# Optimization experiments

Measured on AMD Instinct MI355X. Metric: run time of the kernel, lower is better.

Reference implementation:

```python
import jax, jax.numpy as jnp
import numpy as np
from jax import lax

EPS = 1e-5  # BatchNorm eps (torch default)


def _bn_relu_conv3x3_s2(x, bn_w, bn_b, bn_m, bn_v, w, b):
    # eval-mode BatchNorm2d -> ReLU -> conv3x3 stride 2 pad 1 (NCHW)
    inv = bn_w / jnp.sqrt(bn_v + EPS)
    y = x * inv[None, :, None, None] + (bn_b - bn_m * inv)[None, :, None, None]
    y = jax.nn.relu(y)
    y = lax.conv_general_dilated(y, w, window_strides=(2, 2),
                                 padding=((1, 1), (1, 1)),
                                 dimension_numbers=("NCHW", "OIHW", "NCHW"))
    return y + b[None, :, None, None]


def _avgpool2x2(x):
    B, C, H, W = x.shape
    return x.reshape(B, C, H // 2, 2, W // 2, 2).mean(axis=(3, 5))


def setup_inputs() -> dict:
    key = jax.random.key(0)
    ks = jax.random.split(key, 24)
    C, C3 = 128, 128 // 3
    d = {"x": jax.random.normal(ks[0], (8, C, 96, 96), jnp.float32)}
    for i, p in enumerate(["f", "g", "h"]):
        base = 1 + i * 6
        d[p + "_bn_w"] = jax.random.uniform(ks[base], (C,), jnp.float32, 0.5, 1.5)
        d[p + "_bn_b"] = jax.random.normal(ks[base + 1], (C,), jnp.float32) * 0.1
        d[p + "_bn_m"] = jax.random.normal(ks[base + 2], (C,), jnp.float32) * 0.1
        d[p + "_bn_v"] = jax.random.uniform(ks[base + 3], (C,), jnp.float32, 0.5, 1.5)
        d[p + "_w"] = jax.random.normal(ks[base + 4], (C, C, 3, 3), jnp.float32) * (1.0 / np.sqrt(9 * C))
        d[p + "_b"] = jax.random.normal(ks[base + 5], (C,), jnp.float32) * 0.01
    d["se_cw"] = jax.random.normal(ks[19], (C3, 2 * C), jnp.float32) * (1.0 / np.sqrt(2 * C))
    d["se_cb"] = jax.random.normal(ks[20], (C3,), jnp.float32) * 0.01
    d["se_uw"] = jax.random.normal(ks[21], (C, C3), jnp.float32) * (1.0 / np.sqrt(C3))
    d["se_ub"] = jax.random.normal(ks[22], (C,), jnp.float32) * 0.01
    d["gamma"] = jax.random.normal(ks[23], (1,), jnp.float32) * 0.5
    return d


def reference(x, f_bn_w, f_bn_b, f_bn_m, f_bn_v, f_w, f_b,
              g_bn_w, g_bn_b, g_bn_m, g_bn_v, g_w, g_b,
              h_bn_w, h_bn_b, h_bn_m, h_bn_v, h_w, h_b,
              se_cw, se_cb, se_uw, se_ub, gamma):
    B, C, H, W = x.shape
    left = _avgpool2x2(x)  # isPrimary=False branch -> [B,C,H/2,W/2]

    f = _bn_relu_conv3x3_s2(x, f_bn_w, f_bn_b, f_bn_m, f_bn_v, f_w, f_b)
    g = _bn_relu_conv3x3_s2(x, g_bn_w, g_bn_b, g_bn_m, g_bn_v, g_w, g_b)
    h = _bn_relu_conv3x3_s2(x, h_bn_w, h_bn_b, h_bn_m, h_bn_v, h_w, h_b)

    Ho, Wo = f.shape[2], f.shape[3]
    N = Ho * Wo
    ff = f.reshape(B, C, N)
    gg = g.reshape(B, C, N)
    hh = h.reshape(B, C, N)

    # s = softmax over last axis of f^T g : [B, N, N]
    scores = jnp.einsum("bcn,bcm->bnm", ff, gg)
    attn = jax.nn.softmax(scores, axis=2)
    s = jnp.einsum("bcn,bnm->bcm", hh, attn).reshape(B, C, Ho, Wo)
    s = gamma[0] * s

    # CompetitiveSE: global-avg x and s -> concat(2C) -> ReLU/1x1(C//3) -> ReLU/1x1(C)
    wx = x.mean(axis=(2, 3))          # [B, C]
    ws = s.mean(axis=(2, 3))          # [B, C]
    wcat = jnp.concatenate([wx, ws], axis=1)  # [B, 2C]
    se = jax.nn.relu(wcat) @ se_cw.T + se_cb
    se = jax.nn.relu(se) @ se_uw.T + se_ub    # [B, C]

    return (left + s) * (1.0 + se[:, :, None, None])
```

## Files before the change

kernel.cpp:

```cpp
#include <hip/hip_runtime.h>
#include <hip/hip_bf16.h>

#define B_   8
#define C_   128
#define H_   96
#define W_   96
#define HP_  98
#define HO_  48
#define N_   2304
#define K_CONV 1152
#define PLANE_IN  9216
#define TOT_OUT (B_*C_*N_)

typedef __attribute__((ext_vector_type(8))) short          s16x8;
typedef __attribute__((ext_vector_type(8))) unsigned short u16x8;
typedef __attribute__((ext_vector_type(4))) unsigned short u16x4;
typedef __attribute__((ext_vector_type(4))) float          f32x4;

#define SW(row, q)   (((row) << 6) + ((((q) ^ (((row) >> 1) & 3))) << 4))
#define SW8(row, q)  (((row) << 7) + ((((q) ^ ((row) & 7))) << 4))
#define SW16(row, q) (((row) << 8) + ((((q) ^ ((row) & 15))) << 4))

__device__ __forceinline__ ushort f2bf(float f) {
  __hip_bfloat16 h = __float2bfloat16(f);
  return *reinterpret_cast<ushort*>(&h);
}

__device__ __forceinline__ float block_reduce_sum_256(float v) {
  #pragma unroll
  for (int o = 32; o > 0; o >>= 1) v += __shfl_down(v, o, 64);
  __shared__ float r[4];
  int lane = threadIdx.x & 63, wv = threadIdx.x >> 6;
  if (lane == 0) r[wv] = v;
  __syncthreads();
  float s = 0.f;
  if (threadIdx.x == 0) s = r[0] + r[1] + r[2] + r[3];
  __syncthreads();
  return s;
}

__global__ void k_prep(const float* __restrict__ w0, const float* __restrict__ b0,
                       const float* __restrict__ m0, const float* __restrict__ v0,
                       const float* __restrict__ w1, const float* __restrict__ b1,
                       const float* __restrict__ m1, const float* __restrict__ v1,
                       const float* __restrict__ w2, const float* __restrict__ b2,
                       const float* __restrict__ m2, const float* __restrict__ v2,
                       float* __restrict__ inv, float* __restrict__ beta) {
  int p = blockIdx.x, c = threadIdx.x;
  const float* w = (p == 0 ? w0 : p == 1 ? w1 : w2);
  const float* bb = (p == 0 ? b0 : p == 1 ? b1 : b2);
  const float* m = (p == 0 ? m0 : p == 1 ? m1 : m2);
  const float* v = (p == 0 ? v0 : p == 1 ? v1 : v2);
  if (c < C_) {
    float iv = w[c] / sqrtf(v[c] + 1e-5f);
    inv[p * 128 + c] = iv;
    beta[p * 128 + c] = bb[c] - m[c] * iv;
  }
}

__global__ __launch_bounds__(256) void k_prep_w(const float* __restrict__ w0,
                                                const float* __restrict__ w1,
                                                const float* __restrict__ w2,
                                                ushort* __restrict__ o0,
                                                ushort* __restrict__ o1,
                                                ushort* __restrict__ o2) {
  int p = blockIdx.y;
  const float* w = (p == 0 ? w0 : p == 1 ? w1 : w2);
  ushort* wb = (p == 0 ? o0 : p == 1 ? o1 : o2);
  int id = blockIdx.x * 256 + threadIdx.x;
  if (id >= C_ * K_CONV) return;
  int co = id / K_CONV, rem = id - co * K_CONV;
  int tap = rem >> 7, ci = rem & 127;
  wb[id] = f2bf(w[co * K_CONV + ci * 9 + tap]);
}

__global__ __launch_bounds__(256) void k_prep_y(const float* __restrict__ x,
                                                const float* __restrict__ pinv,
                                                const float* __restrict__ pbeta,
                                                ushort* __restrict__ y0,
                                                ushort* __restrict__ y1,
                                                ushort* __restrict__ y2) {
  const int h1 = blockIdx.x, b = blockIdx.y, t = threadIdx.x;
  ushort* ys[3] = {y0 + (size_t)b * HP_ * HP_ * C_,
                   y1 + (size_t)b * HP_ * HP_ * C_,
                   y2 + (size_t)b * HP_ * HP_ * C_};
  u16x8 zer = (u16x8)0;
  if (h1 == 0 || h1 == HP_ - 1) {
    for (int p = 0; p < 3; ++p)
      for (int g = t; g < HP_ * C_ / 8; g += 256)
        *(u16x8*)(ys[p] + (size_t)h1 * HP_ * C_ + g * 8) = zer;
    return;
  }
  __shared__ float xs[128][97];
  const int h = h1 - 1;
  const float* xb = x + (size_t)b * C_ * PLANE_IN + h * W_;
  for (int id = t; id < 128 * 24; id += 256) {
    int ci = id / 24, w4 = id - ci * 24;
    float4 v = *(const float4*)(xb + (size_t)ci * PLANE_IN + w4 * 4);
    xs[ci][w4 * 4 + 0] = v.x; xs[ci][w4 * 4 + 1] = v.y;
    xs[ci][w4 * 4 + 2] = v.z; xs[ci][w4 * 4 + 3] = v.w;
  }
  __syncthreads();
  if (t < 32) {
    int side = t >> 4, cg = t & 15;
    for (int p = 0; p < 3; ++p)
      *(u16x8*)(ys[p] + ((size_t)h1 * HP_ + (side ? HP_ - 1 : 0)) * C_ + cg * 8) = zer;
  }
  for (int p = 0; p < 3; ++p) {
    const float* inv = pinv + p * 128;
    const float* bet = pbeta + p * 128;
    for (int g = t; g < 96 * 16; g += 256) {
      int wdx = g >> 4, cg = g & 15;
      u16x8 o;
      #pragma unroll
      for (int k = 0; k < 8; ++k) {
        int ci = cg * 8 + k;
        o[k] = f2bf(fmaxf(xs[ci][wdx] * inv[ci] + bet[ci], 0.f));
      }
      *(u16x8*)(ys[p] + ((size_t)h1 * HP_ + (wdx + 1)) * C_ + cg * 8) = o;
    }
  }
}

__global__ __launch_bounds__(256) void k_meanx(const float* __restrict__ x,
                                               float* __restrict__ wcat) {
  int bc = blockIdx.x;
  const float* p = x + (size_t)bc * PLANE_IN;
  float s = 0.f;
  for (int i = threadIdx.x; i < PLANE_IN; i += 256) s += p[i];
  s = block_reduce_sum_256(s);
  if (threadIdx.x == 0) {
    int b = bc >> 7, c = bc & 127;
    wcat[b * 256 + c] = fmaxf(s * (1.f / PLANE_IN), 0.f);
  }
}

__global__ __launch_bounds__(256) void k_conv3(
    const ushort* __restrict__ y0, const ushort* __restrict__ y1, const ushort* __restrict__ y2,
    const ushort* __restrict__ w0, const ushort* __restrict__ w1, const ushort* __restrict__ w2,
    const float* __restrict__ bi0, const float* __restrict__ bi1, const float* __restrict__ bi2,
    ushort* __restrict__ fo, ushort* __restrict__ go, ushort* __restrict__ ho) {
  __shared__ __align__(16) char smem[16384];
  char* As = smem;
  char* Bs = smem + 8192;
  const int br = blockIdx.y, b = blockIdx.z, n0 = blockIdx.x * 64;
  const int t = threadIdx.x, l = t & 63, w = t >> 6;
  const ushort* yb = (br == 0 ? y0 : br == 1 ? y1 : y2) + (size_t)b * HP_ * HP_ * C_;
  const ushort* wb = (br == 0 ? w0 : br == 1 ? w1 : w2);
  const float* bias = (br == 0 ? bi0 : br == 1 ? bi1 : bi2);
  const int pos = t >> 2, q = t & 3;
  const int n_glob = n0 + pos;
  const int oh = n_glob / HO_, ow = n_glob - oh * HO_;
  const int mh = (w & 1) * 64, nh = (w >> 1) * 32;
  f32x4 acc[4][2];
  #pragma unroll
  for (int i = 0; i < 4; ++i)
    #pragma unroll
    for (int j = 0; j < 2; ++j) acc[i][j] = (f32x4)0.f;

  for (int k0 = 0; k0 < K_CONV; k0 += 32) {
    int tap = k0 >> 7, ci0 = k0 & 127;
    int kh = tap / 3, kw = tap - kh * 3;
    #pragma unroll
    for (int g2 = 0; g2 < 2; ++g2) {
      int g = t + g2 * 256, row = g >> 2, qq = g & 3;
      u16x8 d = *(const u16x8*)(wb + row * K_CONV + k0 + qq * 8);
      *(u16x8*)(As + SW(row, qq)) = d;
    }
    {
      int h1 = 2 * oh + kh, w1 = 2 * ow + kw;
      u16x8 d = *(const u16x8*)(yb + ((size_t)h1 * HP_ + w1) * C_ + ci0 + q * 8);
      *(u16x8*)(Bs + SW(pos, q)) = d;
    }
    __syncthreads();
    s16x8 af[4], bf[2];
    #pragma unroll
    for (int i = 0; i < 4; ++i) {
      int r = mh + i * 16 + (l & 15);
      af[i] = *(const s16x8*)(As + SW(r, (l >> 4)));
    }
    #pragma unroll
    for (int j = 0; j < 2; ++j) {
      int r = nh + j * 16 + (l & 15);
      bf[j] = *(const s16x8*)(Bs + SW(r, (l >> 4)));
    }
    #pragma unroll
    for (int i = 0; i < 4; ++i)
      #pragma unroll
      for (int j = 0; j < 2; ++j)
        acc[i][j] = __builtin_amdgcn_mfma_f32_16x16x32_bf16(af[i], bf[j], acc[i][j], 0, 0, 0);
    __syncthreads();
  }

  if (br < 2) {
    ushort* out = (br == 0) ? fo : go;
    ushort* tb = (ushort*)smem;
    #pragma unroll
    for (int i = 0; i < 4; ++i) {
      int co4 = mh + i * 16 + (l >> 4) * 4;
      float4 bi = *(const float4*)&bias[co4];
      float bia[4] = {bi.x, bi.y, bi.z, bi.w};
      #pragma unroll
      for (int j = 0; j < 2; ++j) {
        int pp = nh + j * 16 + (l & 15);
        #pragma unroll
        for (int r = 0; r < 4; ++r)
          tb[pp * 128 + co4 + r] = f2bf(acc[i][j][r] + bia[r]);
      }
    }
    __syncthreads();
    #pragma unroll
    for (int it = 0; it < 4; ++it) {
      int g = t + it * 256;
      int row = g >> 4, gg = g & 15;
      u16x8 d = *(const u16x8*)(tb + row * 128 + gg * 8);
      *(u16x8*)(out + ((size_t)b * N_ + n0 + row) * C_ + gg * 8) = d;
    }
  } else {
    ushort* tb = (ushort*)smem;
    #pragma unroll
    for (int i = 0; i < 4; ++i) {
      int co4 = mh + i * 16 + (l >> 4) * 4;
      float4 bi = *(const float4*)&bias[co4];
      float bia[4] = {bi.x, bi.y, bi.z, bi.w};
      #pragma unroll
      for (int j = 0; j < 2; ++j) {
        int pp = nh + j * 16 + (l & 15);
        #pragma unroll
        for (int r = 0; r < 4; ++r)
          tb[(co4 + r) * 64 + pp] = f2bf(acc[i][j][r] + bia[r]);
      }
    }
    __syncthreads();
    for (int g = t; g < 1024; g += 256) {
      int co = g >> 3, off2 = (g & 7) * 8;
      u16x8 d = *(const u16x8*)(tb + co * 64 + off2);
      *(u16x8*)(ho + ((size_t)b * C_ + co) * N_ + n0 + off2) = d;
    }
  }
}

__global__ __launch_bounds__(256) void k_stats(const ushort* __restrict__ f,
                                               const ushort* __restrict__ g,
                                               float2* __restrict__ pstats) {
  __shared__ __align__(16) char smem[32768];
  const int blk = blockIdx.x;
  const int b = blk & 7, t2 = blk >> 3;
  const int n0 = (t2 % 36) * 64, mz = t2 / 36;
  const int t = threadIdx.x, l = t & 63, w = t >> 6, lo = l & 15, quad = l >> 4;
  const ushort* fb = f + (size_t)b * N_ * C_;
  const ushort* gb = g + (size_t)b * N_ * C_;
  s16x8 af[4];
  #pragma unroll
  for (int ks = 0; ks < 4; ++ks)
    af[ks] = *(const s16x8*)(fb + (size_t)(n0 + w * 16 + lo) * C_ + (ks * 4 + quad) * 8);
  float mloc[4], lloc[4];
  #pragma unroll
  for (int r = 0; r < 4; ++r) { mloc[r] = -1e30f; lloc[r] = 0.f; }
  const int m_beg = mz * 576;

  u16x8 st[4];
  #pragma unroll
  for (int it = 0; it < 4; ++it) {
    int G = t + it * 256, row = G >> 4, g16 = G & 15;
    st[it] = *(const u16x8*)(gb + (size_t)(m_beg + row) * C_ + g16 * 8);
  }
  #pragma unroll
  for (int it = 0; it < 4; ++it) {
    int G = t + it * 256, row = G >> 4, g16 = G & 15;
    *(u16x8*)(smem + SW16(row, g16)) = st[it];
  }
  __syncthreads();

  #pragma unroll
  for (int i9 = 0; i9 < 9; ++i9) {
    char* gs = smem + ((i9 & 1) << 14);
    if (i9 < 8) {
      int m0n = m_beg + (i9 + 1) * 64;
      #pragma unroll
      for (int it = 0; it < 4; ++it) {
        int G = t + it * 256, row = G >> 4, g16 = G & 15;
        st[it] = *(const u16x8*)(gb + (size_t)(m0n + row) * C_ + g16 * 8);
      }
    }
    f32x4 acc[4];
    #pragma unroll
    for (int j = 0; j < 4; ++j) acc[j] = (f32x4)0.f;
    __builtin_amdgcn_s_setprio(1);
    #pragma unroll
    for (int ks = 0; ks < 4; ++ks)
      #pragma unroll
      for (int j = 0; j < 4; ++j) {
        s16x8 bf = *(const s16x8*)(gs + SW16(j * 16 + lo, ks * 4 + quad));
        acc[j] = __builtin_amdgcn_mfma_f32_16x16x32_bf16(af[ks], bf, acc[j], 0, 0, 0);
      }
    __builtin_amdgcn_s_setprio(0);
    #pragma unroll
    for (int r = 0; r < 4; ++r) {
      float vmax = fmaxf(fmaxf(acc[0][r], acc[1][r]), fmaxf(acc[2][r], acc[3][r]));
      float mn = fmaxf(mloc[r], vmax);
      lloc[r] = lloc[r] * __expf(mloc[r] - mn) +
                __expf(acc[0][r] - mn) + __expf(acc[1][r] - mn) +
                __expf(acc[2][r] - mn) + __expf(acc[3][r] - mn);
      mloc[r] = mn;
    }
    if (i9 < 8) {
      char* gn = smem + (((i9 + 1) & 1) << 14);
      #pragma unroll
      for (int it = 0; it < 4; ++it) {
        int G = t + it * 256, row = G >> 4, g16 = G & 15;
        *(u16x8*)(gn + SW16(row, g16)) = st[it];
      }
    }
    __syncthreads();
  }
  #pragma unroll
  for (int r = 0; r < 4; ++r) {
    #pragma unroll
    for (int o = 1; o < 16; o <<= 1) {
      float mo = __shfl_xor(mloc[r], o, 64);
      float lo2 = __shfl_xor(lloc[r], o, 64);
      float mn = fmaxf(mloc[r], mo);
      lloc[r] = lloc[r] * __expf(mloc[r] - mn) + lo2 * __expf(mo - mn);
      mloc[r] = mn;
    }
  }
  if (lo == 0) {
    #pragma unroll
    for (int r = 0; r < 4; ++r)
      pstats[((size_t)mz * B_ + b) * N_ + n0 + w * 16 + quad * 4 + r] =
          make_float2(mloc[r], lloc[r]);
  }
}

__global__ __launch_bounds__(256) void k_stats_red(const float2* __restrict__ p,
                                                   float* __restrict__ astat) {
  int idx = blockIdx.x * 256 + threadIdx.x;
  if (idx >= B_ * N_) return;
  float mx = -1e30f, ls = 0.f;
  #pragma unroll
  for (int z = 0; z < 4; ++z) {
    float2 s = p[(size_t)z * B_ * N_ + idx];
    float mn = fmaxf(mx, s.x);
    ls = ls * __expf(mx - mn) + s.y * __expf(s.x - mn);
    mx = mn;
  }
  astat[idx] = -mx - __logf(ls);
}

__global__ __launch_bounds__(256) void k_attn_out(const ushort* __restrict__ f,
                                                  const ushort* __restrict__ g,
                                                  const ushort* __restrict__ h,
                                                  const float* __restrict__ astat,
                                                  float* __restrict__ spart) {
  __shared__ __align__(16) char smem[35072];
  char* gs = smem;
  char* pTb = smem + 16384;
  const int blk = blockIdx.x;
  const int b = blk & 7, t2 = blk >> 3;
  const int m0 = (t2 % 36) * 64, nz = t2 / 36;
  const int t = threadIdx.x, l = t & 63, w = t >> 6, lo = l & 15, quad = l >> 4;
  const ushort* fb = f + (size_t)b * N_ * C_;
  const ushort* gb = g + (size_t)b * N_ * C_;
  const ushort* hb = h + (size_t)b * C_ * N_;
  const float* ab = astat + (size_t)b * N_;
  #pragma unroll
  for (int it = 0; it < 4; ++it) {
    int G = t + it * 256, row = G >> 4, g16 = G & 15;
    *(u16x8*)(gs + SW16(row, g16)) = *(const u16x8*)(gb + (size_t)(m0 + row) * C_ + g16 * 8);
  }
  f32x4 accs[2][4];
  #pragma unroll
  for (int i = 0; i < 2; ++i)
    #pragma unroll
    for (int j = 0; j < 4; ++j) accs[i][j] = (f32x4)0.f;
  const int n_beg = nz * 576;

  s16x8 af[2][4];
  s16x8 ahc[2][2];
  float ax[2][4];

  auto LOAD_AF = [&](int i, int p) {
    int nb = n_beg + i * 64;
    #pragma unroll
    for (int ks = 0; ks < 4; ++ks)
      af[p][ks] = *(const s16x8*)(fb + (size_t)(nb + w * 16 + lo) * C_ + (ks * 4 + quad) * 8);
    float4 av = *(const float4*)(ab + nb + w * 16 + quad * 4);
    ax[p][0] = av.x; ax[p][1] = av.y; ax[p][2] = av.z; ax[p][3] = av.w;
  };
  auto LOAD_AH = [&](int i) {
    int nb = n_beg + i * 64;
    #pragma unroll
    for (int ii = 0; ii < 2; ++ii)
      #pragma unroll
      for (int ks = 0; ks < 2; ++ks)
        ahc[ii][ks] = *(const s16x8*)(hb + (size_t)((2 * w + ii) * 16 + lo) * N_ + nb + (ks * 4 + quad) * 8);
  };
  auto QKEXP = [&](int p) {
    char* pT = pTb + (p << 13);
    f32x4 sc[4];
    #pragma unroll
    for (int j = 0; j < 4; ++j) sc[j] = (f32x4)0.f;
    __builtin_amdgcn_s_setprio(1);
    #pragma unroll
    for (int ks = 0; ks < 4; ++ks)
      #pragma unroll
      for (int j = 0; j < 4; ++j) {
        s16x8 bg = *(const s16x8*)(gs + SW16(j * 16 + lo, ks * 4 + quad));
        sc[j] = __builtin_amdgcn_mfma_f32_16x16x32_bf16(af[p][ks], bg, sc[j], 0, 0, 0);
      }
    __builtin_amdgcn_s_setprio(0);
    const int nl = w * 16 + quad * 4;
    #pragma unroll
    for (int j = 0; j < 4; ++j) {
      u16x4 pv;
      #pragma unroll
      for (int r = 0; r < 4; ++r)
        pv[r] = f2bf(__expf(sc[j][r] + ax[p][r]));
      *(u16x4*)(pT + SW8(j * 16 + lo, nl >> 3) + (nl & 7) * 2) = pv;
    }
  };
  auto PV = [&](int p) {
    char* pT = pTb + (p << 13);
    __builtin_amdgcn_s_setprio(1);
    #pragma unroll
    for (int ks = 0; ks < 2; ++ks)
      #pragma unroll
      for (int j = 0; j < 4; ++j) {
        s16x8 bp = *(const s16x8*)(pT + SW8(j * 16 + lo, ks * 4 + quad));
        accs[0][j] = __builtin_amdgcn_mfma_f32_16x16x32_bf16(ahc[0][ks], bp, accs[0][j], 0, 0, 0);
        accs[1][j] = __builtin_amdgcn_mfma_f32_16x16x32_bf16(ahc[1][ks], bp, accs[1][j], 0, 0, 0);
      }
    __builtin_amdgcn_s_setprio(0);
  };

  LOAD_AF(0, 0);
  LOAD_AH(0);
  __syncthreads();
  QKEXP(0);
  LOAD_AF(1, 1);
  #pragma unroll
  for (int i9 = 0; i9 < 9; ++i9) {
    __syncthreads();
    PV(i9 & 1);
    if (i9 < 8) {
      LOAD_AH(i9 + 1);
      QKEXP((i9 + 1) & 1);
      if (i9 < 7) LOAD_AF(i9 + 2, i9 & 1);
    }
  }
  __syncthreads();
  float* ss = (float*)smem;
  #pragma unroll
  for (int i = 0; i < 2; ++i) {
    int c0 = (2 * w + i) * 16 + quad * 4;
    #pragma unroll
    for (int j = 0; j < 4; ++j) {
      int m = j * 16 + lo;
      #pragma unroll
      for (int r = 0; r < 4; ++r)
        ss[(c0 + r) * 68 + m] = accs[i][j][r];
    }
  }
  __syncthreads();
  float* outp = spart + (size_t)nz * TOT_OUT + (size_t)b * C_ * N_ + m0;
  #pragma unroll
  for (int it = 0; it < 8; ++it) {
    int idx = t + it * 256;
    int c = idx >> 4, mq = idx & 15;
    float4 v = *(const float4*)&ss[c * 68 + mq * 4];
    *(float4*)&outp[(size_t)c * N_ + mq * 4] = v;
  }
}

__global__ __launch_bounds__(256) void k_sred(const float* __restrict__ spart,
                                              const float* __restrict__ gammap,
                                              float* __restrict__ sbuf) {
  int idx = blockIdx.x * 256 + threadIdx.x;
  if (idx >= TOT_OUT) return;
  float s = spart[idx] + spart[(size_t)TOT_OUT + idx] +
            spart[2 * (size_t)TOT_OUT + idx] + spart[3 * (size_t)TOT_OUT + idx];
  sbuf[idx] = gammap[0] * s;
}

__global__ __launch_bounds__(256) void k_means(const float* __restrict__ s,
                                               float* __restrict__ wcat) {
  int bc = blockIdx.x;
  const float* p = s + (size_t)bc * N_;
  float sm = 0.f;
  for (int i = threadIdx.x; i < N_; i += 256) sm += p[i];
  sm = block_reduce_sum_256(sm);
  if (threadIdx.x == 0) {
    int b = bc >> 7, c = bc & 127;
    wcat[b * 256 + 128 + c] = fmaxf(sm * (1.f / N_), 0.f);
  }
}

__global__ __launch_bounds__(128) void k_se(const float* __restrict__ wcat,
                                            const float* __restrict__ cw,
                                            const float* __restrict__ cb,
                                            const float* __restrict__ uw,
                                            const float* __restrict__ ub,
                                            float* __restrict__ se) {
  const int b = blockIdx.x, t = threadIdx.x;
  __shared__ float wc[256];
  __shared__ float s1[42];
  wc[t] = wcat[b * 256 + t];
  wc[128 + t] = wcat[b * 256 + 128 + t];
  __syncthreads();
  if (t < 42) {
    float a = cb[t];
    const float* r = cw + (size_t)t * 256;
    for (int k = 0; k < 256; ++k) a += wc[k] * r[k];
    s1[t] = fmaxf(a, 0.f);
  }
  __syncthreads();
  {
    float a = ub[t];
    const float* r = uw + (size_t)t * 42;
    for (int j = 0; j < 42; ++j) a += s1[j] * r[j];
    se[b * 128 + t] = a;
  }
}

__global__ __launch_bounds__(256) void k_final(const float* __restrict__ x,
                                               const float* __restrict__ s,
                                               const float* __restrict__ se,
                                               float* __restrict__ out) {
  int idx = blockIdx.x * 256 + threadIdx.x;
  if (idx >= TOT_OUT) return;
  int m  = idx % N_;
  int bc = idx / N_;
  int oh = m / HO_, ow = m - oh * HO_;
  const float* xp = x + (size_t)bc * PLANE_IN;
  int ih = oh * 2, iw = ow * 2;
  float l = 0.25f * (xp[ih * W_ + iw] + xp[ih * W_ + iw + 1] +
                     xp[(ih + 1) * W_ + iw] + xp[(ih + 1) * W_ + iw + 1]);
  out[idx] = (l + s[idx]) * (1.f + se[bc]);
}

extern "C" void kernel_launch(void* const* d_in, const int* in_sizes, int n_in,
                              void* d_out, int out_size, void* d_ws, size_t ws_size,
                              hipStream_t stream) {
  (void)in_sizes; (void)n_in; (void)out_size; (void)ws_size;
  const float* x    = (const float*)d_in[0];
  const float* bnw[3] = {(const float*)d_in[1],  (const float*)d_in[7],  (const float*)d_in[13]};
  const float* bnb[3] = {(const float*)d_in[2],  (const float*)d_in[8],  (const float*)d_in[14]};
  const float* bnm[3] = {(const float*)d_in[3],  (const float*)d_in[9],  (const float*)d_in[15]};
  const float* bnv[3] = {(const float*)d_in[4],  (const float*)d_in[10], (const float*)d_in[16]};
  const float* cw_[3] = {(const float*)d_in[5],  (const float*)d_in[11], (const float*)d_in[17]};
  const float* cbb[3] = {(const float*)d_in[6],  (const float*)d_in[12], (const float*)d_in[18]};
  const float* secw = (const float*)d_in[19];
  const float* secb = (const float*)d_in[20];
  const float* seuw = (const float*)d_in[21];
  const float* seub = (const float*)d_in[22];
  const float* gamma = (const float*)d_in[23];
  float* out = (float*)d_out;

  char* ws = (char*)d_ws;
  size_t off = 0;
  auto alloc = [&](size_t bytes) -> char* {
    char* p = ws + off;
    off = (off + bytes + 255) & ~(size_t)255;
    return p;
  };
  ushort* yp[3];
  for (int p = 0; p < 3; ++p) yp[p] = (ushort*)alloc((size_t)B_ * HP_ * HP_ * C_ * 2);
  ushort* wb[3];
  for (int p = 0; p < 3; ++p) wb[p] = (ushort*)alloc((size_t)C_ * K_CONV * 2);
  ushort* fbuf = (ushort*)alloc((size_t)B_ * N_ * C_ * 2);
  ushort* gbuf = (ushort*)alloc((size_t)B_ * N_ * C_ * 2);
  ushort* hbuf = (ushort*)alloc((size_t)B_ * C_ * N_ * 2);
  float2* pstats = (float2*)alloc((size_t)4 * B_ * N_ * 8);
  float*  astat  = (float*)alloc((size_t)B_ * N_ * 4);
  float*  spart = (float*)alloc((size_t)4 * TOT_OUT * 4);
  float*  sbuf = (float*)alloc((size_t)TOT_OUT * 4);
  float*  wcat = (float*)alloc(B_ * 256 * 4);
  float*  sebuf = (float*)alloc(B_ * 128 * 4);
  float*  pinv  = (float*)alloc(3 * 128 * 4);
  float*  pbeta = (float*)alloc(3 * 128 * 4);

  k_prep<<<3, 128, 0, stream>>>(bnw[0], bnb[0], bnm[0], bnv[0],
                                bnw[1], bnb[1], bnm[1], bnv[1],
                                bnw[2], bnb[2], bnm[2], bnv[2], pinv, pbeta);
  k_prep_w<<<dim3((C_ * K_CONV + 255) / 256, 3), 256, 0, stream>>>(
      cw_[0], cw_[1], cw_[2], wb[0], wb[1], wb[2]);
  k_prep_y<<<dim3(HP_, B_), 256, 0, stream>>>(x, pinv, pbeta, yp[0], yp[1], yp[2]);
  k_meanx<<<B_ * C_, 256, 0, stream>>>(x, wcat);

  k_conv3<<<dim3(N_ / 64, 3, B_), 256, 0, stream>>>(yp[0], yp[1], yp[2],
                                                    wb[0], wb[1], wb[2],
                                                    cbb[0], cbb[1], cbb[2],
                                                    fbuf, gbuf, hbuf);

  k_stats<<<1152, 256, 0, stream>>>(fbuf, gbuf, pstats);
  k_stats_red<<<(B_ * N_ + 255) / 256, 256, 0, stream>>>(pstats, astat);
  k_attn_out<<<1152, 256, 0, stream>>>(fbuf, gbuf, hbuf, astat, spart);
  k_sred<<<(TOT_OUT + 255) / 256, 256, 0, stream>>>(spart, gamma, sbuf);

  k_means<<<B_ * C_, 256, 0, stream>>>(sbuf, wcat);
  k_se<<<B_, 128, 0, stream>>>(wcat, secw, secb, seuw, seub, sebuf);

  k_final<<<(TOT_OUT + 255) / 256, 256, 0, stream>>>(x, sbuf, sebuf, out);
}
```

Baseline: 292.2 us.

## Double-buffer conv loads, fold gamma into h, atomically reduce attention partials

The conv kernel now prefetches the next K-slice into registers while MFMAs run on the current LDS buffer, and uses ping-pong LDS buffers so each step needs only one barrier. Gamma is applied to h inside the conv epilogue. The four nz-split partial outputs of attn_out are accumulated with float atomicAdd straight into a zeroed sbuf, which removes the spart buffer and the k_sred pass. The cost is a memset plus uncoalesced scalar atomics, and a float summation order that is no longer deterministic.

```diff
diff --git a/kernel.cpp b/kernel.cpp
--- a/kernel.cpp
+++ b/kernel.cpp
@@ -139,15 +139,15 @@
     const ushort* __restrict__ y0, const ushort* __restrict__ y1, const ushort* __restrict__ y2,
     const ushort* __restrict__ w0, const ushort* __restrict__ w1, const ushort* __restrict__ w2,
     const float* __restrict__ bi0, const float* __restrict__ bi1, const float* __restrict__ bi2,
+    const float* __restrict__ gammap,
     ushort* __restrict__ fo, ushort* __restrict__ go, ushort* __restrict__ ho) {
-  __shared__ __align__(16) char smem[16384];
-  char* As = smem;
-  char* Bs = smem + 8192;
+  __shared__ __align__(16) char smem[24576];
   const int br = blockIdx.y, b = blockIdx.z, n0 = blockIdx.x * 64;
   const int t = threadIdx.x, l = t & 63, w = t >> 6;
   const ushort* yb = (br == 0 ? y0 : br == 1 ? y1 : y2) + (size_t)b * HP_ * HP_ * C_;
   const ushort* wb = (br == 0 ? w0 : br == 1 ? w1 : w2);
   const float* bias = (br == 0 ? bi0 : br == 1 ? bi1 : bi2);
+  const float gm = (br == 2) ? gammap[0] : 1.f;
   const int pos = t >> 2, q = t & 3;
   const int n_glob = n0 + pos;
   const int oh = n_glob / HO_, ow = n_glob - oh * HO_;
@@ -158,37 +158,48 @@
     #pragma unroll
     for (int j = 0; j < 2; ++j) acc[i][j] = (f32x4)0.f;
 
-  for (int k0 = 0; k0 < K_CONV; k0 += 32) {
+  u16x8 sA0, sA1, sB;
+  auto LD = [&](int k0) {
     int tap = k0 >> 7, ci0 = k0 & 127;
     int kh = tap / 3, kw = tap - kh * 3;
-    #pragma unroll
-    for (int g2 = 0; g2 < 2; ++g2) {
-      int g = t + g2 * 256, row = g >> 2, qq = g & 3;
-      u16x8 d = *(const u16x8*)(wb + row * K_CONV + k0 + qq * 8);
-      *(u16x8*)(As + SW(row, qq)) = d;
-    }
-    {
-      int h1 = 2 * oh + kh, w1 = 2 * ow + kw;
-      u16x8 d = *(const u16x8*)(yb + ((size_t)h1 * HP_ + w1) * C_ + ci0 + q * 8);
-      *(u16x8*)(Bs + SW(pos, q)) = d;
-    }
-    __syncthreads();
+    sA0 = *(const u16x8*)(wb + (t >> 2) * K_CONV + k0 + (t & 3) * 8);
+    sA1 = *(const u16x8*)(wb + ((t >> 2) + 64) * K_CONV + k0 + (t & 3) * 8);
+    int h1 = 2 * oh + kh, w1 = 2 * ow + kw;
+    sB = *(const u16x8*)(yb + ((size_t)h1 * HP_ + w1) * C_ + ci0 + q * 8);
+  };
+  auto ST = [&](char* As, char* Bs) {
+    *(u16x8*)(As + SW(t >> 2, t & 3)) = sA0;
+    *(u16x8*)(As + SW((t >> 2) + 64, t & 3)) = sA1;
+    *(u16x8*)(Bs + SW(pos, q)) = sB;
+  };
+
+  LD(0);
+  ST(smem, smem + 16384);
+  __syncthreads();
+  for (int s = 0; s < 36; ++s) {
+    char* Asc = smem + ((s & 1) << 13);
+    char* Bsc = smem + 16384 + ((s & 1) << 12);
+    if (s < 35) LD((s + 1) * 32);
     s16x8 af[4], bf[2];
     #pragma unroll
     for (int i = 0; i < 4; ++i) {
       int r = mh + i * 16 + (l & 15);
-      af[i] = *(const s16x8*)(As + SW(r, (l >> 4)));
+      af[i] = *(const s16x8*)(Asc + SW(r, (l >> 4)));
     }
     #pragma unroll
     for (int j = 0; j < 2; ++j) {
       int r = nh + j * 16 + (l & 15);
-      bf[j] = *(const s16x8*)(Bs + SW(r, (l >> 4)));
-    }
+      bf[j] = *(const s16x8*)(Bsc + SW(r, (l >> 4)));
+    }
+    __builtin_amdgcn_s_setprio(1);
     #pragma unroll
     for (int i = 0; i < 4; ++i)
       #pragma unroll
       for (int j = 0; j < 2; ++j)
         acc[i][j] = __builtin_amdgcn_mfma_f32_16x16x32_bf16(af[i], bf[j], acc[i][j], 0, 0, 0);
+    __builtin_amdgcn_s_setprio(0);
+    if (s < 35)
+      ST(smem + (((s + 1) & 1) << 13), smem + 16384 + (((s + 1) & 1) << 12));
     __syncthreads();
   }
 
@@ -228,7 +239,7 @@
         int pp = nh + j * 16 + (l & 15);
         #pragma unroll
         for (int r = 0; r < 4; ++r)
-          tb[(co4 + r) * 64 + pp] = f2bf(acc[i][j][r] + bia[r]);
+          tb[(co4 + r) * 64 + pp] = f2bf((acc[i][j][r] + bia[r]) * gm);
       }
     }
     __syncthreads();
@@ -352,8 +363,8 @@
                                                   const ushort* __restrict__ g,
                                                   const ushort* __restrict__ h,
                                                   const float* __restrict__ astat,
-                                                  float* __restrict__ spart) {
-  __shared__ __align__(16) char smem[35072];
+                                                  float* __restrict__ sbuf) {
+  __shared__ __align__(16) char smem[32768];
   char* gs = smem;
   char* pTb = smem + 16384;
   const int blk = blockIdx.x;
@@ -449,8 +460,7 @@
       if (i9 < 7) LOAD_AF(i9 + 2, i9 & 1);
     }
   }
-  __syncthreads();
-  float* ss = (float*)smem;
+  float* outp = sbuf + (size_t)b * C_ * N_ + m0;
   #pragma unroll
   for (int i = 0; i < 2; ++i) {
     int c0 = (2 * w + i) * 16 + quad * 4;
@@ -459,28 +469,9 @@
       int m = j * 16 + lo;
       #pragma unroll
       for (int r = 0; r < 4; ++r)
-        ss[(c0 + r) * 68 + m] = accs[i][j][r];
-    }
-  }
-  __syncthreads();
-  float* outp = spart + (size_t)nz * TOT_OUT + (size_t)b * C_ * N_ + m0;
-  #pragma unroll
-  for (int it = 0; it < 8; ++it) {
-    int idx = t + it * 256;
-    int c = idx >> 4, mq = idx & 15;
-    float4 v = *(const float4*)&ss[c * 68 + mq * 4];
-    *(float4*)&outp[(size_t)c * N_ + mq * 4] = v;
-  }
-}
-
-__global__ __launch_bounds__(256) void k_sred(const float* __restrict__ spart,
-                                              const float* __restrict__ gammap,
-                                              float* __restrict__ sbuf) {
-  int idx = blockIdx.x * 256 + threadIdx.x;
-  if (idx >= TOT_OUT) return;
-  float s = spart[idx] + spart[(size_t)TOT_OUT + idx] +
-            spart[2 * (size_t)TOT_OUT + idx] + spart[3 * (size_t)TOT_OUT + idx];
-  sbuf[idx] = gammap[0] * s;
+        atomicAdd(&outp[(size_t)(c0 + r) * N_ + m], accs[i][j][r]);
+    }
+  }
 }
 
 __global__ __launch_bounds__(256) void k_means(const float* __restrict__ s,
@@ -573,12 +564,13 @@
   ushort* hbuf = (ushort*)alloc((size_t)B_ * C_ * N_ * 2);
   float2* pstats = (float2*)alloc((size_t)4 * B_ * N_ * 8);
   float*  astat  = (float*)alloc((size_t)B_ * N_ * 4);
-  float*  spart = (float*)alloc((size_t)4 * TOT_OUT * 4);
   float*  sbuf = (float*)alloc((size_t)TOT_OUT * 4);
   float*  wcat = (float*)alloc(B_ * 256 * 4);
   float*  sebuf = (float*)alloc(B_ * 128 * 4);
   float*  pinv  = (float*)alloc(3 * 128 * 4);
   float*  pbeta = (float*)alloc(3 * 128 * 4);
+
+  hipMemsetAsync(sbuf, 0, (size_t)TOT_OUT * 4, stream);
 
   k_prep<<<3, 128, 0, stream>>>(bnw[0], bnb[0], bnm[0], bnv[0],
                                 bnw[1], bnb[1], bnm[1], bnv[1],
@@ -590,13 +582,12 @@
 
   k_conv3<<<dim3(N_ / 64, 3, B_), 256, 0, stream>>>(yp[0], yp[1], yp[2],
                                                     wb[0], wb[1], wb[2],
-                                                    cbb[0], cbb[1], cbb[2],
+                                                    cbb[0], cbb[1], cbb[2], gamma,
                                                     fbuf, gbuf, hbuf);
 
   k_stats<<<1152, 256, 0, stream>>>(fbuf, gbuf, pstats);
   k_stats_red<<<(B_ * N_ + 255) / 256, 256, 0, stream>>>(pstats, astat);
-  k_attn_out<<<1152, 256, 0, stream>>>(fbuf, gbuf, hbuf, astat, spart);
-  k_sred<<<(TOT_OUT + 255) / 256, 256, 0, stream>>>(spart, gamma, sbuf);
+  k_attn_out<<<1152, 256, 0, stream>>>(fbuf, gbuf, hbuf, astat, sbuf);
 
   k_means<<<B_ * C_, 256, 0, stream>>>(sbuf, wcat);
   k_se<<<B_, 128, 0, stream>>>(wcat, secw, secb, seuw, seub, sebuf);
```

After: 289.5 us. Within noise of the previous version (-0.9%).
